# Optimization experiments

Measured on AMD Instinct MI355X. Metric: run time of the kernel, lower is better.

The kernel has to match this reference:

```python
import jax, jax.numpy as jnp
import numpy as np

B, L, N, C = 16, 12, 512, 3
SEQ = 12
FFT = SEQ // 2 + 1
EMB, ID_EMB, HID = 64, 64, 128
RC, DC, SC, EC = 32, 32, 256, 512
OUT, KS, BLOCKS, LAYERS = 12, 2, 4, 2
TID, DIW = 288, 7
K_SUB = 20
A_COEF = 0.5
NLAYERS = BLOCKS * LAYERS
DILATIONS = [1, 2] * BLOCKS
RECEPTIVE = 13  # 1 + blocks*(1+2) with kernel_size=2, layers=2


def setup_inputs() -> dict:
    key = jax.random.key(0)
    ks = jax.random.split(key, 20)
    r = jax.random.normal
    return {
        "history_data": jax.random.uniform(ks[0], (B, L, N, C), jnp.float32),
        "start_w": r(ks[1], (RC, 2)) * 0.1, "start_b": jnp.zeros((RC,)),
        "filt_w": r(ks[2], (NLAYERS, DC, RC, KS)) * 0.1, "filt_b": jnp.zeros((NLAYERS, DC)),
        "gate_w": r(ks[3], (NLAYERS, DC, RC, KS)) * 0.1, "gate_b": jnp.zeros((NLAYERS, DC)),
        "skip_w": r(ks[4], (NLAYERS, SC, DC)) * 0.1, "skip_b": jnp.zeros((NLAYERS, SC)),
        "gconv_w": r(ks[5], (NLAYERS, RC, 5 * DC)) * 0.1, "gconv_b": jnp.zeros((NLAYERS, RC)),
        "end1_w": r(ks[6], (EC, SC)) * 0.05, "end1_b": jnp.zeros((EC,)),
        "end2_w": r(ks[7], (OUT, EC)) * 0.05, "end2_b": jnp.zeros((OUT,)),
        "Ex1": r(ks[8], (FFT, EMB)) * 0.1,
        "node1": r(ks[9], (N, ID_EMB)) * 0.1,
        "Wd": r(ks[10], (N, EMB + ID_EMB + 2 * SEQ, HID)) * 0.05,
        "Wxabs": r(ks[11], (HID, HID)) * 0.05,
        "TiD_emb": r(ks[12], (TID, SEQ)) * 0.1,
        "DiW_emb": r(ks[13], (DIW, SEQ)) * 0.1,
        "nodevec1": r(ks[14], (N, EMB)) * 0.1,
        "nodevec2": r(ks[15], (EMB, N)) * 0.1,
    }


def conv1x1(x, w, b):
    # x: [B,C,N,L], w: [O,C] -> [B,O,N,L]
    return jnp.einsum('bcnl,oc->bonl', x, w) + b[None, :, None, None]


def tconv(x, w, b, d):
    # dilated (1,2) temporal conv; w: [O,C,2]
    lo = x[..., : x.shape[-1] - d]
    hi = x[..., d:]
    y = jnp.einsum('bcnl,oc->bonl', lo, w[..., 0]) + jnp.einsum('bcnl,oc->bonl', hi, w[..., 1])
    return y + b[None, :, None, None]


def nconv(x, A):
    if A.ndim == 2:
        return jnp.einsum('bcvl,vw->bcwl', x, A)
    return jnp.einsum('bcvl,bvw->bcwl', x, A)


def gcn(x, supports, w, b):
    out = [x]
    for A in supports:  # order = 2 hops per support
        x1 = nconv(x, A)
        out.append(x1)
        out.append(nconv(x1, A))
    return conv1x1(jnp.concatenate(out, axis=1), w, b)  # dropout is identity in eval


def _forward(history_data, start_w, start_b, filt_w, filt_b, gate_w, gate_b,
             skip_w, skip_b, gconv_w, gconv_b, end1_w, end1_b, end2_w, end2_b,
             Ex1, node1, Wd, Wxabs, TiD_emb, DiW_emb, nodevec1, nodevec2):
    inp = jnp.transpose(history_data, (0, 3, 2, 1))[:, 0:2]          # [B,2,N,L]
    x = jnp.pad(inp, ((0, 0), (0, 0), (0, 0), (RECEPTIVE - L, 0)))   # left-pad time
    x = conv1x1(x, start_w, start_b)                                  # [B,RC,N,13]

    # self-adaptive graph (Graph WaveNet)
    gwadp = jax.nn.softmax(jax.nn.relu(nodevec1 @ nodevec2), axis=1)  # [N,N]

    # dynamic frequency-domain graph
    xn1 = inp[:, 0, :, -SEQ:]                                         # [B,N,SEQ]
    freq = jnp.abs(jnp.fft.rfft(xn1, axis=-1))                        # [B,N,FFT]
    e = jnp.einsum('bnf,fk->bnk', freq, Ex1)                          # [B,N,EMB]
    e = jnp.concatenate([e, jnp.broadcast_to(node1, (B, N, ID_EMB))], axis=2)
    T_D = TiD_emb[(history_data[:, -1, :, 1] * TID).astype(jnp.int32)]  # [B,N,SEQ]
    D_W = DiW_emb[(history_data[:, -1, :, 2] * DIW).astype(jnp.int32)]  # [B,N,SEQ]
    e = jnp.concatenate([e, T_D, D_W], axis=2)                        # [B,N,EMB+ID+2*SEQ]
    adp = jnp.einsum('bne,nek->bnk', e, Wd)                           # per-node projection
    mu = adp.mean(axis=(1, 2), keepdims=True)
    var = adp.var(axis=(1, 2), keepdims=True)
    adp = (adp - mu) / jnp.sqrt(var + 1e-8)                           # LayerNorm [N,HID], no affine
    adj = jax.nn.relu(jnp.einsum('bnk,kj,bmj->bnm', adp, Wxabs, adp))  # [B,N,N]
    noise = jax.random.uniform(jax.random.key(42), adj.shape) * 0.01
    _, idx = jax.lax.top_k(adj + noise, K_SUB)                        # [B,N,K] row-wise topk
    mask = jnp.zeros_like(adj).at[
        jnp.arange(B)[:, None, None], jnp.arange(N)[None, :, None], idx].set(1.0)
    adj = jax.nn.softmax(adj * mask, axis=2)
    supports = [gwadp, A_COEF * adj]

    skip = None
    bn_scale = 1.0 / np.sqrt(1.0 + 1e-5)  # eval BatchNorm with default running stats
    for i in range(NLAYERS):
        residual = x
        f = jnp.tanh(tconv(residual, filt_w[i], filt_b[i], DILATIONS[i]))
        g = jax.nn.sigmoid(tconv(residual, gate_w[i], gate_b[i], DILATIONS[i]))
        x = f * g
        s = conv1x1(x, skip_w[i], skip_b[i])
        skip = s if skip is None else s + skip[..., -s.shape[-1]:]
        x = gcn(x, supports, gconv_w[i], gconv_b[i])
        x = x + residual[..., -x.shape[-1]:]
        x = x * bn_scale
    x = jax.nn.relu(skip)
    x = jax.nn.relu(conv1x1(x, end1_w, end1_b))
    return conv1x1(x, end2_w, end2_b)  # [B,OUT,N,1]


def reference(history_data, start_w, start_b, filt_w, filt_b, gate_w, gate_b,
              skip_w, skip_b, gconv_w, gconv_b, end1_w, end1_b, end2_w, end2_b,
              Ex1, node1, Wd, Wxabs, TiD_emb, DiW_emb, nodevec1, nodevec2):
    return _forward(history_data, start_w, start_b, filt_w, filt_b, gate_w, gate_b,
                    skip_w, skip_b, gconv_w, gconv_b, end1_w, end1_b, end2_w, end2_b,
                    Ex1, node1, Wd, Wxabs, TiD_emb, DiW_emb, nodevec1, nodevec2)
```

## Files before the change

### kernel.cpp

```cpp
#include <hip/hip_runtime.h>
#include <cstdint>
#include <math.h>

typedef unsigned short ushort_t;
typedef __bf16 bf16x8 __attribute__((ext_vector_type(8)));
typedef float f32x4 __attribute__((ext_vector_type(4)));

#define BNSCALE 0.9999950000374998f

__device__ __forceinline__ ushort_t f2b(float x){
  union { float f; uint32_t u; } v; v.f = x;
  uint32_t u = v.u;
  u = u + 0x7fffu + ((u >> 16) & 1u);
  return (ushort_t)(u >> 16);
}
__device__ __forceinline__ float b2f(ushort_t h){
  union { float f; uint32_t u; } v; v.u = ((uint32_t)h) << 16; return v.f;
}

__device__ __forceinline__ uint32_t rotl32(uint32_t x, int d){ return (x<<d)|(x>>(32-d)); }

__device__ __forceinline__ void threefry2x32(uint32_t& x0, uint32_t& x1){
  const uint32_t ks0=0u, ks1=42u, ks2=42u^0x1BD11BDAu;
  x0+=ks0; x1+=ks1;
  x0+=x1; x1=rotl32(x1,13); x1^=x0;
  x0+=x1; x1=rotl32(x1,15); x1^=x0;
  x0+=x1; x1=rotl32(x1,26); x1^=x0;
  x0+=x1; x1=rotl32(x1, 6); x1^=x0;
  x0+=ks1; x1+=ks2+1u;
  x0+=x1; x1=rotl32(x1,17); x1^=x0;
  x0+=x1; x1=rotl32(x1,29); x1^=x0;
  x0+=x1; x1=rotl32(x1,16); x1^=x0;
  x0+=x1; x1=rotl32(x1,24); x1^=x0;
  x0+=ks2; x1+=ks0+2u;
  x0+=x1; x1=rotl32(x1,13); x1^=x0;
  x0+=x1; x1=rotl32(x1,15); x1^=x0;
  x0+=x1; x1=rotl32(x1,26); x1^=x0;
  x0+=x1; x1=rotl32(x1, 6); x1^=x0;
  x0+=ks0; x1+=ks1+3u;
  x0+=x1; x1=rotl32(x1,17); x1^=x0;
  x0+=x1; x1=rotl32(x1,29); x1^=x0;
  x0+=x1; x1=rotl32(x1,16); x1^=x0;
  x0+=x1; x1=rotl32(x1,24); x1^=x0;
  x0+=ks1; x1+=ks2+4u;
  x0+=x1; x1=rotl32(x1,13); x1^=x0;
  x0+=x1; x1=rotl32(x1,15); x1^=x0;
  x0+=x1; x1=rotl32(x1,26); x1^=x0;
  x0+=x1; x1=rotl32(x1, 6); x1^=x0;
  x0+=ks2; x1+=ks0+5u;
}

__global__ void k_start(const float* __restrict__ hist, const float* __restrict__ sw,
                        const float* __restrict__ sb, float* __restrict__ x){
  int idx = blockIdx.x*256 + threadIdx.x;
  int n = idx & 511; int r = idx >> 9;
  int o = r & 31; int r2 = r >> 5;
  int t = r2 % 13; int b = r2 / 13;
  float acc = sb[o];
  if (t > 0){
    const float* h = hist + ((size_t)(b*12 + (t-1))*512 + n)*3;
    acc += h[0]*sw[o*2+0] + h[1]*sw[o*2+1];
  }
  x[(((size_t)(b*13 + t)*32 + o))*512 + n] = acc;
}

__global__ void k_gw_mm(const float* __restrict__ nv1, const float* __restrict__ nv2,
                        float* __restrict__ gw){
  int idx = blockIdx.x*256+threadIdx.x;
  int w = idx & 511, v = idx >> 9;
  float acc=0.f;
  #pragma unroll
  for (int k=0;k<64;k++) acc += nv1[v*64+k]*nv2[k*512+w];
  gw[idx]=acc;
}

__global__ void k_gw_sm(float* __restrict__ gw){
  int v = blockIdx.x; int tid=threadIdx.x;
  float a0 = fmaxf(gw[v*512+tid],0.f), a1=fmaxf(gw[v*512+256+tid],0.f);
  __shared__ float red[256];
  red[tid]=fmaxf(a0,a1); __syncthreads();
  for(int s=128;s>0;s>>=1){ if(tid<s) red[tid]=fmaxf(red[tid],red[tid+s]); __syncthreads(); }
  float m = red[0]; __syncthreads();
  float e0=expf(a0-m), e1=expf(a1-m);
  red[tid]=e0+e1; __syncthreads();
  for(int s=128;s>0;s>>=1){ if(tid<s) red[tid]+=red[tid+s]; __syncthreads(); }
  float inv = 1.0f/red[0];
  gw[v*512+tid]=e0*inv; gw[v*512+256+tid]=e1*inv;
}

__global__ void k_embed(const float* __restrict__ hist, const float* __restrict__ Ex1,
                        const float* __restrict__ node1, const float* __restrict__ TiD,
                        const float* __restrict__ DiW, float* __restrict__ e){
  const float c12[12] = {1.f, 0.8660254037844387f, 0.5f, 0.f, -0.5f, -0.8660254037844387f,
                         -1.f, -0.8660254037844387f, -0.5f, 0.f, 0.5f, 0.8660254037844387f};
  const float s12[12] = {0.f, -0.5f, -0.8660254037844387f, -1.f, -0.8660254037844387f, -0.5f,
                         0.f, 0.5f, 0.8660254037844387f, 1.f, 0.8660254037844387f, 0.5f};
  int row = blockIdx.x; int b = row >> 9; int n = row & 511;
  int tid = threadIdx.x;
  __shared__ float fr[7];
  if (tid < 7){
    float re=0.f, im=0.f;
    for (int l=0;l<12;l++){
      float v = hist[((size_t)(b*12+l)*512+n)*3];
      int idx = (tid*l) % 12;
      re += v*c12[idx]; im += v*s12[idx];
    }
    fr[tid]=sqrtf(re*re+im*im);
  }
  __syncthreads();
  float* er = e + (size_t)row*152;
  float acc=0.f;
  #pragma unroll
  for (int f=0;f<7;f++) acc += fr[f]*Ex1[f*64+tid];
  er[tid]=acc;
  er[64+tid]=node1[n*64+tid];
  if (tid<12){
    int it = (int)(hist[((size_t)(b*12+11)*512+n)*3+1]*288.0f);
    int id = (int)(hist[((size_t)(b*12+11)*512+n)*3+2]*7.0f);
    er[128+tid]=TiD[it*12+tid];
    er[140+tid]=DiW[id*12+tid];
  }
}

__global__ void k_adp(const float* __restrict__ e, const float* __restrict__ Wd,
                      float* __restrict__ adp){
  int n = blockIdx.x; int tid = threadIdx.x;
  __shared__ float es[16][152];
  for (int idx = tid; idx < 16*152; idx += 128){
    int r = idx / 152, q = idx - r*152;
    es[r][q] = e[((size_t)(r*512+n))*152 + q];
  }
  __syncthreads();
  const float* w = Wd + (size_t)n*152*128;
  float acc[16];
  #pragma unroll
  for (int r=0;r<16;r++) acc[r]=0.f;
  for (int q = 0; q < 152; q++){
    float wv = w[q*128 + tid];
    #pragma unroll
    for (int r = 0; r < 16; r++) acc[r] += es[r][q]*wv;
  }
  #pragma unroll
  for (int r=0;r<16;r++) adp[((size_t)(r*512+n))*128 + tid] = acc[r];
}

__global__ void k_lnp1(const float* __restrict__ adp, float* __restrict__ part){
  int blk = blockIdx.x; int tid = threadIdx.x;
  const float* p = adp + (size_t)(blk>>4)*65536 + (size_t)(blk&15)*4096;
  float s=0.f, s2=0.f;
  for (int i=tid;i<4096;i+=256){ float v=p[i]; s+=v; s2+=v*v; }
  __shared__ float rs[256], rs2[256];
  rs[tid]=s; rs2[tid]=s2; __syncthreads();
  for(int k=128;k>0;k>>=1){ if(tid<k){rs[tid]+=rs[tid+k]; rs2[tid]+=rs2[tid+k];} __syncthreads(); }
  if(tid==0){ part[blk*2]=rs[0]; part[blk*2+1]=rs2[0]; }
}

__global__ void k_lnp2(const float* __restrict__ part, float* __restrict__ stats){
  int tid = threadIdx.x;
  int b = tid >> 4, c = tid & 15;
  float s = part[tid*2], s2 = part[tid*2+1];
  #pragma unroll
  for (int off=8; off>=1; off>>=1){ s += __shfl_down(s,off); s2 += __shfl_down(s2,off); }
  if (c==0){
    float mu = s/65536.f; float var = s2/65536.f - mu*mu;
    stats[b*2]=mu; stats[b*2+1]=rsqrtf(var+1e-8f);
  }
}

__global__ void k_xw(const float* __restrict__ adp, const float* __restrict__ Wx,
                     const float* __restrict__ stats, float* __restrict__ t){
  int row=blockIdx.x; int tid=threadIdx.x; int b=row>>9;
  __shared__ float as[128];
  as[tid]=(adp[(size_t)row*128+tid]-stats[2*b])*stats[2*b+1];
  __syncthreads();
  float acc=0.f;
  #pragma unroll 8
  for(int k=0;k<128;k++) acc += as[k]*Wx[k*128+tid];
  t[(size_t)row*128+tid]=acc;
}

__global__ __launch_bounds__(256) void k_adjmm(const float* __restrict__ T,
                        const float* __restrict__ P, const float* __restrict__ stats,
                        float* __restrict__ adj){
  int b = blockIdx.z;
  int n0 = blockIdx.y*32, m0 = blockIdx.x*64;
  const float* Tb = T + (size_t)b*512*128;
  const float* Pb = P + (size_t)b*512*128;
  float mu = stats[2*b], isig = stats[2*b+1];
  __shared__ float Ts[32][33];
  __shared__ float Ps[64][33];
  int tid=threadIdx.x; int tx=tid&15, ty=tid>>4;
  float acc[2][4]={};
  for(int k0=0;k0<128;k0+=32){
    for(int q=0;q<4;q++){ int idx=tid+q*256; int r=idx>>5, kk=idx&31; Ts[r][kk]=Tb[(size_t)(n0+r)*128+k0+kk]; }
    for(int q=0;q<8;q++){ int idx=tid+q*256; int r=idx>>5, kk=idx&31; Ps[r][kk]=(Pb[(size_t)(m0+r)*128+k0+kk]-mu)*isig; }
    __syncthreads();
    #pragma unroll
    for(int kk=0;kk<32;kk++){
      float t0=Ts[ty][kk], t1=Ts[ty+16][kk];
      float p0=Ps[tx*4+0][kk], p1=Ps[tx*4+1][kk], p2=Ps[tx*4+2][kk], p3=Ps[tx*4+3][kk];
      acc[0][0]+=t0*p0; acc[0][1]+=t0*p1; acc[0][2]+=t0*p2; acc[0][3]+=t0*p3;
      acc[1][0]+=t1*p0; acc[1][1]+=t1*p1; acc[1][2]+=t1*p2; acc[1][3]+=t1*p3;
    }
    __syncthreads();
  }
  for(int i2=0;i2<2;i2++){
    int n=n0+ty+16*i2;
    float4 o4=make_float4(fmaxf(acc[i2][0],0.f),fmaxf(acc[i2][1],0.f),
                          fmaxf(acc[i2][2],0.f),fmaxf(acc[i2][3],0.f));
    *(float4*)&adj[((size_t)b*512+n)*512+m0+tx*4]=o4;
  }
}

__global__ void k_topk(float* __restrict__ adj){
  const int row = blockIdx.x;
  const int tid = threadIdx.x;
  const uint32_t halfn = 2097152u;
  float a[8], v[8];
  const bool lowhalf = row < 4096;
  #pragma unroll
  for(int k=0;k<8;k++){
    int m = k*64+tid;
    uint32_t i = (uint32_t)row*512u + (uint32_t)m;
    uint32_t c0 = lowhalf ? i : i - halfn;
    uint32_t x0=c0, x1=c0+halfn;
    threefry2x32(x0,x1);
    uint32_t bits = lowhalf ? x0 : x1;
    float u = __uint_as_float((bits>>9)|0x3f800000u)-1.0f;
    a[k]=adj[(size_t)row*512+m];
    v[k]=a[k]+0.01f*u;
  }
  unsigned selmask=0u;
  for(int it=0; it<20; it++){
    float best=-1e30f; int bi=0x7fffffff;
    #pragma unroll
    for(int k=0;k<8;k++){
      if(!((selmask>>k)&1u)){
        int m=k*64+tid;
        if(v[k]>best || (v[k]==best && m<bi)){best=v[k]; bi=m;}
      }
    }
    #pragma unroll
    for(int off=32; off>=1; off>>=1){
      float ov=__shfl_xor(best,off); int oi=__shfl_xor(bi,off);
      if(ov>best || (ov==best && oi<bi)){best=ov; bi=oi;}
    }
    if((bi&63)==tid) selmask |= 1u<<(bi>>6);
  }
  float M=0.f;
  #pragma unroll
  for(int k=0;k<8;k++) if((selmask>>k)&1u) M=fmaxf(M,a[k]);
  #pragma unroll
  for(int off=32;off>=1;off>>=1) M=fmaxf(M,__shfl_xor(M,off));
  float S=0.f;
  #pragma unroll
  for(int k=0;k<8;k++) S += expf((((selmask>>k)&1u)? a[k]:0.f) - M);
  #pragma unroll
  for(int off=32;off>=1;off>>=1) S += __shfl_xor(S,off);
  float inv = 0.5f/S;
  #pragma unroll
  for(int k=0;k<8;k++){
    int m=k*64+tid;
    adj[(size_t)row*512+m] = expf((((selmask>>k)&1u)? a[k]:0.f)-M)*inv;
  }
}

__global__ void k_split(const float* __restrict__ src, ushort_t* __restrict__ hi,
                        ushort_t* __restrict__ lo, int count){
  int i = blockIdx.x*256+threadIdx.x;
  if (i < count){
    float v = src[i];
    ushort_t h = f2b(v);
    hi[i] = h;
    lo[i] = f2b(v - b2f(h));
  }
}

__global__ void k_splitT(const float* __restrict__ src, long sBS,
                         ushort_t* __restrict__ hi, long hBS, int hRS,
                         ushort_t* __restrict__ lo, long lBS, int lRS){
  int b = blockIdx.z;
  int c0 = blockIdx.x*32, r0 = blockIdx.y*32;
  __shared__ float tile[32][33];
  int tx = threadIdx.x & 31, ty = threadIdx.x >> 5;
  for (int q = 0; q < 4; q++)
    tile[ty+q*8][tx] = src[b*sBS + (size_t)(r0+ty+q*8)*512 + c0+tx];
  __syncthreads();
  for (int q = 0; q < 4; q++){
    int cc = c0+ty+q*8, rr = r0+tx;
    float v = tile[tx][ty+q*8];
    ushort_t h = f2b(v);
    hi[b*hBS + (size_t)cc*hRS + rr] = h;
    lo[b*lBS + (size_t)cc*lRS + rr] = f2b(v - b2f(h));
  }
}

__global__ __launch_bounds__(256,2) void k_pow(
    const ushort_t* __restrict__ Ah, const ushort_t* __restrict__ Al, long aBS,
    const ushort_t* __restrict__ Bh, const ushort_t* __restrict__ Bl, long bBS,
    ushort_t* __restrict__ Ch, ushort_t* __restrict__ Cl, long cBS){
  __shared__ __align__(16) ushort_t At[5120];
  __shared__ __align__(16) ushort_t Bt[5120];
  const int b = blockIdx.z;
  const int r0 = blockIdx.x*64, n0 = blockIdx.y*64;
  const int tid = threadIdx.x;
  const int w = tid >> 6, l = tid & 63, lr = l & 15, kg = l >> 4;
  const int wr = w & 1, wc = w >> 1;
  const int ra = tid >> 2, ca = (tid & 3)*8;
  const ushort_t* Ahp = Ah + (long)b*aBS + (long)(r0+ra)*512 + ca;
  const ushort_t* Alp = Al + (long)b*aBS + (long)(r0+ra)*512 + ca;
  const ushort_t* Bhp = Bh + (long)b*bBS + (long)(n0+ra)*512 + ca;
  const ushort_t* Blp = Bl + (long)b*bBS + (long)(n0+ra)*512 + ca;
  f32x4 acc[2][2];
  #pragma unroll
  for (int ms=0; ms<2; ms++)
    #pragma unroll
    for (int ns=0; ns<2; ns++) acc[ms][ns] = (f32x4){0.f,0.f,0.f,0.f};
  uint4 pA0,pA1,pB0,pB1;
  #define LDP(K0) { \
    pA0 = *(const uint4*)(Ahp + (K0)); pA1 = *(const uint4*)(Alp + (K0)); \
    pB0 = *(const uint4*)(Bhp + (K0)); pB1 = *(const uint4*)(Blp + (K0)); }
  LDP(0);
  for (int k0 = 0; k0 < 512; k0 += 32){
    __syncthreads();
    *(uint4*)&At[ra*40 + ca]        = pA0;
    *(uint4*)&At[2560 + ra*40 + ca] = pA1;
    *(uint4*)&Bt[ra*40 + ca]        = pB0;
    *(uint4*)&Bt[2560 + ra*40 + ca] = pB1;
    __syncthreads();
    if (k0 + 32 < 512) LDP(k0 + 32);
    bf16x8 ahv[2], alv[2], bhv[2], blv[2];
    #pragma unroll
    for (int ms=0; ms<2; ms++){
      int ar = wr*32 + ms*16 + lr;
      ahv[ms] = *(const bf16x8*)&At[ar*40 + kg*8];
      alv[ms] = *(const bf16x8*)&At[2560 + ar*40 + kg*8];
    }
    #pragma unroll
    for (int ns=0; ns<2; ns++){
      int br = wc*32 + ns*16 + lr;
      bhv[ns] = *(const bf16x8*)&Bt[br*40 + kg*8];
      blv[ns] = *(const bf16x8*)&Bt[2560 + br*40 + kg*8];
    }
    #pragma unroll
    for (int ms=0; ms<2; ms++)
      #pragma unroll
      for (int ns=0; ns<2; ns++){
        acc[ms][ns] = __builtin_amdgcn_mfma_f32_16x16x32_bf16(ahv[ms], bhv[ns], acc[ms][ns], 0, 0, 0);
        acc[ms][ns] = __builtin_amdgcn_mfma_f32_16x16x32_bf16(alv[ms], bhv[ns], acc[ms][ns], 0, 0, 0);
        acc[ms][ns] = __builtin_amdgcn_mfma_f32_16x16x32_bf16(ahv[ms], blv[ns], acc[ms][ns], 0, 0, 0);
      }
  }
  #undef LDP
  #pragma unroll
  for (int ms=0; ms<2; ms++)
    #pragma unroll
    for (int rg=0; rg<4; rg++){
      int r = r0 + wr*32 + ms*16 + kg*4 + rg;
      #pragma unroll
      for (int ns=0; ns<2; ns++){
        int n = n0 + wc*32 + ns*16 + lr;
        float v = acc[ms][ns][rg];
        long ofs = (long)b*cBS + (long)r*512 + n;
        ushort_t hv = f2b(v);
        Ch[ofs] = hv;
        Cl[ofs] = f2b(v - b2f(hv));
      }
    }
}

__global__ __launch_bounds__(256,1) void k_gemms(
    const ushort_t* __restrict__ Afh, const ushort_t* __restrict__ Afl,
    const ushort_t* __restrict__ S0h, const ushort_t* __restrict__ S0l,
    const ushort_t* __restrict__ S1h, const ushort_t* __restrict__ S1l,
    const ushort_t* __restrict__ S2h, const ushort_t* __restrict__ S2l,
    const ushort_t* __restrict__ S3h, const ushort_t* __restrict__ S3l,
    const float* __restrict__ gcw, float* __restrict__ xnew,
    int Mt, int M, int lo){
  __shared__ __align__(16) char smem[51200];
  ushort_t* At = (ushort_t*)smem;
  ushort_t* Bt = (ushort_t*)(smem + 10240);
  float* m32 = (float*)smem;
  float* Wgs = (float*)(smem + 16896);
  const int total = gridDim.x;
  const int chunk = total >> 3;
  const int lid = blockIdx.x;
  const int swz = (lid & 7)*chunk + (lid >> 3);
  const int x = swz % Mt;
  const int rest = swz / Mt;
  const int y = rest & 7;
  const int b = rest >> 3;
  const int n0 = y*64, r0 = x*64;
  const int tid = threadIdx.x;
  const int w = tid >> 6, l = tid & 63, lr = l & 15, kg = l >> 4;
  const int wr = w & 1, wc = w >> 1;
  const int ra = tid >> 2, ca = (tid & 3)*8;
  int arow = r0 + ra; if (arow >= M) arow = M - 1;
  const ushort_t* Ahp = Afh + (long)b*M*512 + (long)arow*512 + ca;
  const ushort_t* Alp = Afl + (long)b*M*512 + (long)arow*512 + ca;
  const int zz = tid >> 6, rb = tid & 63;
  const ushort_t* Bz; const ushort_t* Bzl;
  if (zz == 0){ Bz = S0h; Bzl = S0l; }
  else if (zz == 1){ Bz = S1h; Bzl = S1l; }
  else if (zz == 2){ Bz = S2h + (long)b*262144; Bzl = S2l + (long)b*262144; }
  else { Bz = S3h + (long)b*262144; Bzl = S3l + (long)b*262144; }
  const ushort_t* Bhp = Bz + (long)(n0 + rb)*512;
  const ushort_t* Blp = Bzl + (long)(n0 + rb)*512;

  f32x4 acc[4][2][2];
  #pragma unroll
  for (int z=0; z<4; z++)
    #pragma unroll
    for (int ms=0; ms<2; ms++)
      #pragma unroll
      for (int ns=0; ns<2; ns++) acc[z][ms][ns] = (f32x4){0.f,0.f,0.f,0.f};

  uint4 pA0,pA1,pB0,pB1,pB2,pB3,pB4,pB5,pB6,pB7;
  #define LDG(K0) { \
    pA0 = *(const uint4*)(Ahp + (K0)); pA1 = *(const uint4*)(Alp + (K0)); \
    pB0 = *(const uint4*)(Bhp + (K0));      pB1 = *(const uint4*)(Bhp + (K0) + 8); \
    pB2 = *(const uint4*)(Bhp + (K0) + 16); pB3 = *(const uint4*)(Bhp + (K0) + 24); \
    pB4 = *(const uint4*)(Blp + (K0));      pB5 = *(const uint4*)(Blp + (K0) + 8); \
    pB6 = *(const uint4*)(Blp + (K0) + 16); pB7 = *(const uint4*)(Blp + (K0) + 24); }
  LDG(0);
  for (int k0 = 0; k0 < 512; k0 += 32){
    __syncthreads();
    *(uint4*)&At[ra*40 + ca]        = pA0;
    *(uint4*)&At[2560 + ra*40 + ca] = pA1;
    {
      ushort_t* bb = Bt + zz*5120 + rb*40;
      *(uint4*)&bb[0]  = pB0; *(uint4*)&bb[8]  = pB1;
      *(uint4*)&bb[16] = pB2; *(uint4*)&bb[24] = pB3;
      ushort_t* bl2 = bb + 2560;
      *(uint4*)&bl2[0]  = pB4; *(uint4*)&bl2[8]  = pB5;
      *(uint4*)&bl2[16] = pB6; *(uint4*)&bl2[24] = pB7;
    }
    __syncthreads();
    if (k0 + 32 < 512) LDG(k0 + 32);
    bf16x8 ahv[2], alv[2];
    #pragma unroll
    for (int ms=0; ms<2; ms++){
      int ar = wr*32 + ms*16 + lr;
      ahv[ms] = *(const bf16x8*)&At[ar*40 + kg*8];
      alv[ms] = *(const bf16x8*)&At[2560 + ar*40 + kg*8];
    }
    #pragma unroll
    for (int z=0; z<4; z++){
      #pragma unroll
      for (int ns=0; ns<2; ns++){
        int br = wc*32 + ns*16 + lr;
        bf16x8 bh = *(const bf16x8*)&Bt[z*5120 + br*40 + kg*8];
        bf16x8 bl = *(const bf16x8*)&Bt[z*5120 + 2560 + br*40 + kg*8];
        #pragma unroll
        for (int ms=0; ms<2; ms++){
          acc[z][ms][ns] = __builtin_amdgcn_mfma_f32_16x16x32_bf16(ahv[ms], bh, acc[z][ms][ns], 0, 0, 0);
          acc[z][ms][ns] = __builtin_amdgcn_mfma_f32_16x16x32_bf16(alv[ms], bh, acc[z][ms][ns], 0, 0, 0);
          acc[z][ms][ns] = __builtin_amdgcn_mfma_f32_16x16x32_bf16(ahv[ms], bl, acc[z][ms][ns], 0, 0, 0);
        }
      }
    }
  }
  #undef LDG
  __syncthreads();
  for (int idx = tid; idx < 4096; idx += 256){
    int z = idx >> 10, rem = idx & 1023;
    int c2 = rem >> 5, c = rem & 31;
    Wgs[idx] = gcw[c*160 + (z+1)*32 + c2];
  }
  const int g = tid >> 6, j = tid & 63;
  float outv[32];
  #pragma unroll
  for (int c=0; c<32; c++) outv[c] = 0.f;
  #pragma unroll
  for (int z=0; z<4; z++){
    __syncthreads();
    #pragma unroll
    for (int ms=0; ms<2; ms++)
      #pragma unroll
      for (int ns=0; ns<2; ns++)
        #pragma unroll
        for (int rg=0; rg<4; rg++)
          m32[(wr*32 + ms*16 + kg*4 + rg)*66 + wc*32 + ns*16 + lr] = acc[z][ms][ns][rg];
    __syncthreads();
    if (tid < 128){
      const float* wzT = Wgs + z*1024;
      for (int c2=0; c2<32; c2++){
        float yv = m32[(g*32 + c2)*66 + j];
        const float* wrow = wzT + c2*32;
        #pragma unroll
        for (int c=0; c<32; c++) outv[c] += wrow[c]*yv;
      }
    }
  }
  if (tid < 128 && r0 + g*32 < M){
    int t = (r0 >> 5) + g;
    long ob = ((long)(b*lo + t)*32)*512 + n0 + j;
    #pragma unroll
    for (int c=0; c<32; c++){
      long ofs = ob + (long)c*512;
      xnew[ofs] += outv[c]*BNSCALE;
    }
  }
}

__global__ void k_mix1(const float* __restrict__ x,
    const float* __restrict__ fw, const float* __restrict__ fb,
    const float* __restrict__ gwv, const float* __restrict__ gb,
    const float* __restrict__ gcw, const float* __restrict__ gcb,
    ushort_t* __restrict__ fgh, ushort_t* __restrict__ fgl,
    float* __restrict__ fgL, float* __restrict__ xnew,
    int d, int li, int lo){
  __shared__ float FWs[2048], GWs[2048], W0s[1024];
  __shared__ float fbs[32], gbs[32], gcbs[32];
  int tid = threadIdx.x;
  int t = blockIdx.y, b = blockIdx.z;
  int n = blockIdx.x*256 + tid;
  for (int idx = tid; idx < 2048; idx += 256){ FWs[idx] = fw[idx]; GWs[idx] = gwv[idx]; }
  for (int idx = tid; idx < 1024; idx += 256) W0s[idx] = gcw[(idx>>5)*160 + (idx&31)];
  if (tid < 32){ fbs[tid]=fb[tid]; gbs[tid]=gb[tid]; gcbs[tid]=gcb[tid]; }
  __syncthreads();
  float xv[32], xv2[32], fgv[32];
  const float* xb  = x + ((size_t)(b*li + t)*32)*512 + n;
  const float* xb2 = x + ((size_t)(b*li + t + d)*32)*512 + n;
  #pragma unroll
  for (int c=0;c<32;c++){ xv[c] = xb[(size_t)c*512]; xv2[c] = xb2[(size_t)c*512]; }
  #pragma unroll
  for (int o=0;o<32;o++){
    float f = fbs[o], g = gbs[o];
    #pragma unroll
    for (int c=0;c<32;c++){
      float2 wf = *(const float2*)&FWs[(o*32+c)*2];
      float2 wg = *(const float2*)&GWs[(o*32+c)*2];
      f += xv[c]*wf.x + xv2[c]*wf.y;
      g += xv[c]*wg.x + xv2[c]*wg.y;
    }
    f = fminf(f, 15.f);
    float e2 = __expf(2.f*f);
    float th = (e2 - 1.f)/(e2 + 1.f);
    float sg = 1.f/(1.f + __expf(-g));
    fgv[o] = th*sg;
  }
  size_t rbase = ((size_t)(b*lo + t)*32)*512 + n;
  #pragma unroll
  for (int o=0;o<32;o++){
    float bs = gcbs[o] + xv2[o];
    #pragma unroll
    for (int c=0;c<32;c++) bs += W0s[o*32+c]*fgv[c];
    xnew[rbase + (size_t)o*512] = bs*BNSCALE;
    ushort_t h = f2b(fgv[o]);
    fgh[rbase + (size_t)o*512] = h;
    fgl[rbase + (size_t)o*512] = f2b(fgv[o] - b2f(h));
  }
  if (t == lo-1){
    #pragma unroll
    for (int o=0;o<32;o++) fgL[((size_t)b*32+o)*512 + n] = fgv[o];
  }
}

__global__ void k_skipacc(const float* __restrict__ fgL, const float* __restrict__ sw,
                          const float* __restrict__ sb, float* __restrict__ skip, int init){
  int b = blockIdx.y; int n0 = blockIdx.x*64;
  int tid = threadIdx.x; int col = tid & 63; int q = tid >> 6;
  __shared__ float fgls[32][65];
  for (int idx = tid; idx < 2048; idx += 256){
    int c = idx >> 6, j = idx & 63;
    fgls[c][j] = fgL[((size_t)b*32+c)*512 + n0 + j];
  }
  __syncthreads();
  for (int s = q*64; s < q*64+64; s++){
    float acc = sb[s];
    #pragma unroll
    for (int c = 0; c < 32; c++) acc += sw[s*32+c]*fgls[c][col];
    size_t o = ((size_t)b*256+s)*512 + n0+col;
    skip[o] = init ? acc : skip[o] + acc;
  }
}

__global__ __launch_bounds__(256) void k_end1t(const float* __restrict__ skip,
                        const float* __restrict__ w, const float* __restrict__ bias,
                        float* __restrict__ h){
  int b = blockIdx.z; int e0 = blockIdx.y*32; int n0 = blockIdx.x*64;
  __shared__ float Ws_[32][33];
  __shared__ float Ss_[32][64];
  int tid = threadIdx.x, tx = tid&15, ty = tid>>4;
  float acc[2][4] = {};
  for (int k0 = 0; k0 < 256; k0 += 32){
    for (int q2 = 0; q2 < 4; q2++){ int idx = tid + q2*256; int r = idx>>5, kk = idx&31;
      Ws_[r][kk] = w[(size_t)(e0+r)*256 + k0+kk]; }
    for (int q2 = 0; q2 < 8; q2++){ int idx = tid + q2*256; int r = idx>>6, ww = idx&63;
      Ss_[r][ww] = fmaxf(skip[(size_t)b*131072 + (size_t)(k0+r)*512 + n0+ww], 0.f); }
    __syncthreads();
    #pragma unroll
    for (int kk = 0; kk < 32; kk++){
      float t0 = Ws_[ty][kk], t1 = Ws_[ty+16][kk];
      float4 b4 = *(float4*)&Ss_[kk][tx*4];
      acc[0][0]+=t0*b4.x; acc[0][1]+=t0*b4.y; acc[0][2]+=t0*b4.z; acc[0][3]+=t0*b4.w;
      acc[1][0]+=t1*b4.x; acc[1][1]+=t1*b4.y; acc[1][2]+=t1*b4.z; acc[1][3]+=t1*b4.w;
    }
    __syncthreads();
  }
  for (int i2 = 0; i2 < 2; i2++){
    int e = e0 + ty + 16*i2;
    float bb = bias[e];
    float4 o4 = make_float4(fmaxf(acc[i2][0]+bb,0.f), fmaxf(acc[i2][1]+bb,0.f),
                            fmaxf(acc[i2][2]+bb,0.f), fmaxf(acc[i2][3]+bb,0.f));
    *(float4*)&h[(size_t)b*262144 + (size_t)e*512 + n0 + tx*4] = o4;
  }
}

__global__ void k_end2(const float* __restrict__ h, const float* __restrict__ w,
                       const float* __restrict__ bias, float* __restrict__ out){
  int n = blockIdx.x*256+threadIdx.x; int o=blockIdx.y; int b=blockIdx.z;
  float acc=bias[o];
  const float* hb=h + (size_t)b*262144 + n;
  #pragma unroll 8
  for (int e=0;e<512;e++) acc += w[o*512+e]*hb[(size_t)e*512];
  out[((size_t)b*12+o)*512+n]=acc;
}

extern "C" void kernel_launch(void* const* d_in, const int* in_sizes, int n_in,
                              void* d_out, int out_size, void* d_ws, size_t ws_size,
                              hipStream_t stream) {
  (void)in_sizes; (void)n_in; (void)out_size;
  const float* hist   =(const float*)d_in[0];
  const float* start_w=(const float*)d_in[1];
  const float* start_b=(const float*)d_in[2];
  const float* filt_w =(const float*)d_in[3];
  const float* filt_b =(const float*)d_in[4];
  const float* gate_w =(const float*)d_in[5];
  const float* gate_b =(const float*)d_in[6];
  const float* skip_w =(const float*)d_in[7];
  const float* skip_b =(const float*)d_in[8];
  const float* gconv_w=(const float*)d_in[9];
  const float* gconv_b=(const float*)d_in[10];
  const float* end1_w =(const float*)d_in[11];
  const float* end1_b =(const float*)d_in[12];
  const float* end2_w =(const float*)d_in[13];
  const float* end2_b =(const float*)d_in[14];
  const float* Ex1    =(const float*)d_in[15];
  const float* node1  =(const float*)d_in[16];
  const float* Wd     =(const float*)d_in[17];
  const float* Wxabs  =(const float*)d_in[18];
  const float* TiD    =(const float*)d_in[19];
  const float* DiW    =(const float*)d_in[20];
  const float* nv1    =(const float*)d_in[21];
  const float* nv2    =(const float*)d_in[22];

  char* ws = (char*)d_ws;
  const size_t needed = 83902464;
  if (ws_size < needed) return;

  ushort_t* PtA_hi  = (ushort_t*)(ws + 0);
  ushort_t* PtA_lo  = (ushort_t*)(ws + 524288);
  ushort_t* PtA2_hi = (ushort_t*)(ws + 1048576);
  ushort_t* PtA2_lo = (ushort_t*)(ws + 1572864);
  ushort_t* PtB_hi  = (ushort_t*)(ws + 2097152);
  ushort_t* PtB_lo  = (ushort_t*)(ws + 10485760);
  ushort_t* PtB2_hi = (ushort_t*)(ws + 18874368);
  ushort_t* PtB2_lo = (ushort_t*)(ws + 27262976);
  float*    stats   = (float*)(ws + 35651584);
  float*    part    = (float*)(ws + 35651712);
  float*    skip    = (float*)(ws + 35667968);
  float*    fgL     = (float*)(ws + 44056576);
  ushort_t* fgh     = (ushort_t*)(ws + 45105152);
  ushort_t* fgl     = (ushort_t*)(ws + 51396608);
  float*    xA      = (float*)(ws + 57688064);
  float*    xB      = (float*)(ws + 71319552);
  float*    gwb     = (float*)(ws + 44056576);
  ushort_t* gws_hi  = (ushort_t*)(ws + 45105152);
  ushort_t* gws_lo  = (ushort_t*)(ws + 45629440);
  float*    ebuf    = (float*)(ws + 46153728);
  ushort_t* adjh    = (ushort_t*)(ws + 46153728);
  float*    adp     = (float*)(ws + 51134464);
  float*    xw      = (float*)(ws + 55328768);
  float*    adjb    = (float*)(ws + 59523072);
  ushort_t* adjl    = (ushort_t*)(ws + 76300288);
  float*    hbuf    = (float*)(ws + 45105152);

  k_embed<<<dim3(8192),dim3(64),0,stream>>>(hist,Ex1,node1,TiD,DiW,ebuf);
  k_adp<<<dim3(512),dim3(128),0,stream>>>(ebuf,Wd,adp);
  k_gw_mm<<<dim3(1024),dim3(256),0,stream>>>(nv1,nv2,gwb);
  k_gw_sm<<<dim3(512),dim3(256),0,stream>>>(gwb);
  k_split<<<dim3(1024),dim3(256),0,stream>>>(gwb, gws_hi, gws_lo, 262144);
  k_splitT<<<dim3(16,16,1),dim3(256),0,stream>>>(gwb, 0, PtA_hi, 0, 512, PtA_lo, 0, 512);
  k_pow<<<dim3(8,8,1),dim3(256),0,stream>>>(
      PtA_hi, PtA_lo, 0, gws_hi, gws_lo, 0, PtA2_hi, PtA2_lo, 0);
  k_lnp1<<<dim3(256),dim3(256),0,stream>>>(adp,part);
  k_lnp2<<<dim3(1),dim3(256),0,stream>>>(part,stats);
  k_xw<<<dim3(8192),dim3(128),0,stream>>>(adp,Wxabs,stats,xw);
  k_adjmm<<<dim3(8,16,16),dim3(256),0,stream>>>(xw,adp,stats,adjb);
  k_topk<<<dim3(8192),dim3(64),0,stream>>>(adjb);
  k_splitT<<<dim3(16,16,16),dim3(256),0,stream>>>(adjb, 262144, PtB_hi, 262144, 512,
                                                  PtB_lo, 262144, 512);
  k_split<<<dim3(16384),dim3(256),0,stream>>>(adjb, adjh, adjl, 4194304);
  k_pow<<<dim3(8,8,16),dim3(256),0,stream>>>(
      PtB_hi, PtB_lo, 262144, adjh, adjl, 262144, PtB2_hi, PtB2_lo, 262144);

  k_start<<<dim3(13312),dim3(256),0,stream>>>(hist,start_w,start_b,xA);

  const int lin[8]={13,12,10,9,7,6,4,3};
  const int dil[8]={1,2,1,2,1,2,1,2};
  float* xcur=xA; float* alt=xB;
  for (int i=0;i<8;i++){
    int d=dil[i], li=lin[i], lo=li-d;
    const float* fwp=filt_w+(size_t)i*2048; const float* fbp=filt_b+i*32;
    const float* gwp=gate_w+(size_t)i*2048; const float* gbp=gate_b+i*32;
    const float* swp=skip_w+(size_t)i*8192; const float* sbp=skip_b+i*256;
    const float* gcwp=gconv_w+(size_t)i*5120; const float* gcbp=gconv_b+i*32;
    int M = 32*lo, Mt = (M+63)/64;

    k_mix1<<<dim3(2,lo,16),dim3(256),0,stream>>>(xcur,fwp,fbp,gwp,gbp,gcwp,gcbp,
        fgh,fgl,fgL,alt,d,li,lo);
    k_skipacc<<<dim3(8,16),dim3(256),0,stream>>>(fgL,swp,sbp,skip,(i==0)?1:0);

    if (i < 7){
      k_gemms<<<dim3(Mt*8*16),dim3(256),0,stream>>>(
          fgh, fgl,
          PtA_hi, PtA_lo, PtA2_hi, PtA2_lo, PtB_hi, PtB_lo, PtB2_hi, PtB2_lo,
          gcwp, alt, Mt, M, lo);
    }
    float* tmp=xcur; xcur=alt; alt=tmp;
  }

  k_end1t<<<dim3(8,16,16),dim3(256),0,stream>>>(skip,end1_w,end1_b,hbuf);
  k_end2<<<dim3(2,12,16),dim3(256),0,stream>>>(hbuf,end2_w,end2_b,(float*)d_out);
}
```

Baseline: 1.446 ms.

## Assign one support per wave in gemms and split skipacc across more blocks

The graph-conv GEMM kernel now gives each wave a full 64x64 tile for a single support matrix, instead of splitting the 2x2 tile grid across all four supports. Each wave then reads only its own support's B tile from LDS, which cuts redundant LDS reads, at the cost of more A-fragment registers. In the epilogue, waves take turns writing their accumulators to shared memory. Separately, k_skipacc gets a grid dimension over skip-channel groups, giving 4x more blocks with 16 channels per thread, to raise parallelism.

```diff
diff --git a/kernel.cpp b/kernel.cpp
--- a/kernel.cpp
+++ b/kernel.cpp
@@ -393,12 +393,11 @@
   const int n0 = y*64, r0 = x*64;
   const int tid = threadIdx.x;
   const int w = tid >> 6, l = tid & 63, lr = l & 15, kg = l >> 4;
-  const int wr = w & 1, wc = w >> 1;
   const int ra = tid >> 2, ca = (tid & 3)*8;
   int arow = r0 + ra; if (arow >= M) arow = M - 1;
   const ushort_t* Ahp = Afh + (long)b*M*512 + (long)arow*512 + ca;
   const ushort_t* Alp = Afl + (long)b*M*512 + (long)arow*512 + ca;
-  const int zz = tid >> 6, rb = tid & 63;
+  const int zz = w, rb = l;
   const ushort_t* Bz; const ushort_t* Bzl;
   if (zz == 0){ Bz = S0h; Bzl = S0l; }
   else if (zz == 1){ Bz = S1h; Bzl = S1l; }
@@ -407,13 +406,11 @@
   const ushort_t* Bhp = Bz + (long)(n0 + rb)*512;
   const ushort_t* Blp = Bzl + (long)(n0 + rb)*512;
 
-  f32x4 acc[4][2][2];
-  #pragma unroll
-  for (int z=0; z<4; z++)
-    #pragma unroll
-    for (int ms=0; ms<2; ms++)
-      #pragma unroll
-      for (int ns=0; ns<2; ns++) acc[z][ms][ns] = (f32x4){0.f,0.f,0.f,0.f};
+  f32x4 acc[4][4];
+  #pragma unroll
+  for (int ms=0; ms<4; ms++)
+    #pragma unroll
+    for (int ns=0; ns<4; ns++) acc[ms][ns] = (f32x4){0.f,0.f,0.f,0.f};
 
   uint4 pA0,pA1,pB0,pB1,pB2,pB3,pB4,pB5,pB6,pB7;
   #define LDG(K0) { \
@@ -437,26 +434,23 @@
     }
     __syncthreads();
     if (k0 + 32 < 512) LDG(k0 + 32);
-    bf16x8 ahv[2], alv[2];
-    #pragma unroll
-    for (int ms=0; ms<2; ms++){
-      int ar = wr*32 + ms*16 + lr;
+    bf16x8 ahv[4], alv[4];
+    #pragma unroll
+    for (int ms=0; ms<4; ms++){
+      int ar = ms*16 + lr;
       ahv[ms] = *(const bf16x8*)&At[ar*40 + kg*8];
       alv[ms] = *(const bf16x8*)&At[2560 + ar*40 + kg*8];
     }
     #pragma unroll
-    for (int z=0; z<4; z++){
+    for (int ns=0; ns<4; ns++){
+      int br = ns*16 + lr;
+      bf16x8 bh = *(const bf16x8*)&Bt[w*5120 + br*40 + kg*8];
+      bf16x8 bl = *(const bf16x8*)&Bt[w*5120 + 2560 + br*40 + kg*8];
       #pragma unroll
-      for (int ns=0; ns<2; ns++){
-        int br = wc*32 + ns*16 + lr;
-        bf16x8 bh = *(const bf16x8*)&Bt[z*5120 + br*40 + kg*8];
-        bf16x8 bl = *(const bf16x8*)&Bt[z*5120 + 2560 + br*40 + kg*8];
-        #pragma unroll
-        for (int ms=0; ms<2; ms++){
-          acc[z][ms][ns] = __builtin_amdgcn_mfma_f32_16x16x32_bf16(ahv[ms], bh, acc[z][ms][ns], 0, 0, 0);
-          acc[z][ms][ns] = __builtin_amdgcn_mfma_f32_16x16x32_bf16(alv[ms], bh, acc[z][ms][ns], 0, 0, 0);
-          acc[z][ms][ns] = __builtin_amdgcn_mfma_f32_16x16x32_bf16(ahv[ms], bl, acc[z][ms][ns], 0, 0, 0);
-        }
+      for (int ms=0; ms<4; ms++){
+        acc[ms][ns] = __builtin_amdgcn_mfma_f32_16x16x32_bf16(ahv[ms], bh, acc[ms][ns], 0, 0, 0);
+        acc[ms][ns] = __builtin_amdgcn_mfma_f32_16x16x32_bf16(alv[ms], bh, acc[ms][ns], 0, 0, 0);
+        acc[ms][ns] = __builtin_amdgcn_mfma_f32_16x16x32_bf16(ahv[ms], bl, acc[ms][ns], 0, 0, 0);
       }
     }
   }
@@ -474,13 +468,15 @@
   #pragma unroll
   for (int z=0; z<4; z++){
     __syncthreads();
-    #pragma unroll
-    for (int ms=0; ms<2; ms++)
+    if (w == z){
       #pragma unroll
-      for (int ns=0; ns<2; ns++)
+      for (int ms=0; ms<4; ms++)
         #pragma unroll
-        for (int rg=0; rg<4; rg++)
-          m32[(wr*32 + ms*16 + kg*4 + rg)*66 + wc*32 + ns*16 + lr] = acc[z][ms][ns][rg];
+        for (int ns=0; ns<4; ns++)
+          #pragma unroll
+          for (int rg=0; rg<4; rg++)
+            m32[(ms*16 + kg*4 + rg)*66 + ns*16 + lr] = acc[ms][ns][rg];
+    }
     __syncthreads();
     if (tid < 128){
       const float* wzT = Wgs + z*1024;
@@ -559,7 +555,7 @@
 
 __global__ void k_skipacc(const float* __restrict__ fgL, const float* __restrict__ sw,
                           const float* __restrict__ sb, float* __restrict__ skip, int init){
-  int b = blockIdx.y; int n0 = blockIdx.x*64;
+  int b = blockIdx.z; int sq = blockIdx.y; int n0 = blockIdx.x*64;
   int tid = threadIdx.x; int col = tid & 63; int q = tid >> 6;
   __shared__ float fgls[32][65];
   for (int idx = tid; idx < 2048; idx += 256){
@@ -567,7 +563,8 @@
     fgls[c][j] = fgL[((size_t)b*32+c)*512 + n0 + j];
   }
   __syncthreads();
-  for (int s = q*64; s < q*64+64; s++){
+  int s0 = sq*64 + q*16;
+  for (int s = s0; s < s0+16; s++){
     float acc = sb[s];
     #pragma unroll
     for (int c = 0; c < 32; c++) acc += sw[s*32+c]*fgls[c][col];
@@ -711,7 +708,7 @@
 
     k_mix1<<<dim3(2,lo,16),dim3(256),0,stream>>>(xcur,fwp,fbp,gwp,gbp,gcwp,gcbp,
         fgh,fgl,fgL,alt,d,li,lo);
-    k_skipacc<<<dim3(8,16),dim3(256),0,stream>>>(fgL,swp,sbp,skip,(i==0)?1:0);
+    k_skipacc<<<dim3(8,4,16),dim3(256),0,stream>>>(fgL,swp,sbp,skip,(i==0)?1:0);
 
     if (i < 7){
       k_gemms<<<dim3(Mt*8*16),dim3(256),0,stream>>>(
```

Measured after the change: 1.260 ms. 1.15x faster.
